# Performance work log

Hardware: AMD Instinct MI355X
Metric: run time of the kernel (lower is better)

The kernel has to match this reference:

```python
import jax, jax.numpy as jnp
import numpy as np

RADIUS = 0.2
MAX_SAMPLES = 32  # max_samples_per_query


def ball_query(coords, queries, radius, k):
    """coords: [B,Np,3], queries: [B,Nq,3] -> idxs: [B,Nq,k] (first-k in index order,
    empty slots filled with the first valid index, or 0 if no neighbor -- matches
    the standard PointNet++ CUDA ball_query semantics)."""
    Np = coords.shape[1]
    # squared distances [B, Nq, Np]
    diff = queries[:, :, None, :] - coords[:, None, :, :]
    d2 = jnp.sum(diff * diff, axis=-1)
    mask = d2 < radius * radius
    # keys: point index if in-ball else sentinel Np; smallest k keys = first k valid indices
    keys = jnp.where(mask, jnp.arange(Np, dtype=jnp.int32), Np)
    neg_top, _ = jax.lax.top_k(-keys, k)           # largest of -keys == smallest keys
    sorted_keys = -neg_top                          # [B, Nq, k], ascending
    valid = sorted_keys < Np
    first = jnp.where(valid[..., 0:1], sorted_keys[..., 0:1], 0)
    return jnp.where(valid, sorted_keys, first)


def setup_inputs() -> dict:
    key = jax.random.key(0)
    k1, k2, k3, k4 = jax.random.split(key, 4)
    B, Np, Nq, C, Ct = 4, 8192, 2048, 64, 64
    return {
        "points_coords": jax.random.uniform(k1, (B, Np, 3), dtype=jnp.float32),
        "points_features": jax.random.normal(k2, (B, C, Np), dtype=jnp.float32),
        "points_t_embed": jax.random.normal(k3, (B, Ct, Np), dtype=jnp.float32),
        "queries": jax.random.uniform(k4, (B, Nq, 3), dtype=jnp.float32),
    }


def reference(points_coords, points_features, points_t_embed, queries):
    B, Np, _ = points_coords.shape
    Nq = queries.shape[1]
    K = MAX_SAMPLES
    idxs = ball_query(points_coords, queries, RADIUS, K)          # [B,Nq,K] int32
    flat = idxs.reshape(B, Nq * K)
    # grouped coords: gather along point dim then center on queries -> [B,Nq,K,3]
    grouped_coords = jnp.take_along_axis(points_coords, flat[:, :, None], axis=1)
    grouped_coords = grouped_coords.reshape(B, Nq, K, 3) - queries[:, :, None, :]
    # grouped features: gather channel-first along point dim -> [B,C,Nq,K]
    C = points_features.shape[1]
    grouped_features = jnp.take_along_axis(points_features, flat[:, None, :], axis=2)
    grouped_features = grouped_features.reshape(B, C, Nq, K)
    # use_coords=True: prepend centered coords as channels
    grouped_features = jnp.concatenate(
        [grouped_coords.transpose(0, 3, 1, 2), grouped_features], axis=1)  # [B,3+C,Nq,K]
    # t_embed gather -> [B,Ct,Nq,K]
    Ct = points_t_embed.shape[1]
    t_embed = jnp.take_along_axis(points_t_embed, flat[:, None, :], axis=2)
    t_embed = t_embed.reshape(B, Ct, Nq, K)
    return grouped_features, t_embed
```

## Files before the change

### kernel.cpp

```cpp
#include <hip/hip_runtime.h>

constexpr int kB  = 4;
constexpr int kNp = 8192;
constexpr int kNq = 2048;
constexpr int kK  = 32;
constexpr float kR2 = (float)(0.2 * 0.2);

typedef float v4f __attribute__((ext_vector_type(4)));
typedef int   v4i __attribute__((ext_vector_type(4)));

__global__ __launch_bounds__(256) void coords_soa_kernel(
    const float* __restrict__ coords, float* __restrict__ cb3)
{
    const int t  = blockIdx.x * 256 + threadIdx.x;
    const int b  = t >> 11;
    const int p4 = t & (kNp / 4 - 1);

    const v4f* c4 = (const v4f*)(coords + (size_t)b * kNp * 3 + (size_t)p4 * 12);
    const v4f d0 = c4[0];
    const v4f d1 = c4[1];
    const v4f d2 = c4[2];

    v4f X = {d0.x, d0.w, d1.z, d2.y};
    v4f Y = {d0.y, d1.x, d1.w, d2.z};
    v4f Z = {d0.z, d1.y, d2.x, d2.w};

    float* o = cb3 + (size_t)b * 3 * kNp;
    ((v4f*)(o + 0 * kNp))[p4] = X;
    ((v4f*)(o + 1 * kNp))[p4] = Y;
    ((v4f*)(o + 2 * kNp))[p4] = Z;
}

__global__ __launch_bounds__(256) void ball_query_kernel(
    const float* __restrict__ cb3,
    const float* __restrict__ queries,
    int* __restrict__ idxs,
    float* __restrict__ out)
{
    const int wave = (int)((blockIdx.x * blockDim.x + threadIdx.x) >> 6);
    const int lane = threadIdx.x & 63;
    const int w    = threadIdx.x >> 6;
    const int b    = wave >> 11;
    const int q    = wave & (kNq - 1);

    const float qx = queries[(b * kNq + q) * 3 + 0];
    const float qy = queries[(b * kNq + q) * 3 + 1];
    const float qz = queries[(b * kNq + q) * 3 + 2];

    const float* __restrict__ cbx = cb3 + (size_t)b * 3 * kNp;
    const float* __restrict__ cby = cbx + kNp;
    const float* __restrict__ cbz = cby + kNp;
    const v4f* __restrict__ cbx4 = (const v4f*)cbx;
    const v4f* __restrict__ cby4 = (const v4f*)cby;
    const v4f* __restrict__ cbz4 = (const v4f*)cbz;

    __shared__ int s_idx[4][kK];

    const unsigned long long lt = (1ull << lane) - 1ull;
    int cnt = 0;

    v4f X = cbx4[lane];
    v4f Y = cby4[lane];
    v4f Z = cbz4[lane];

    for (int base = 0; base < kNp; base += 256) {
        const int nvi = (base + 256 < kNp) ? (((base + 256) >> 2) + lane) : lane;
        const v4f Xn = cbx4[nvi];
        const v4f Yn = cby4[nvi];
        const v4f Zn = cbz4[nvi];

        bool in[4];
        unsigned long long m[4];
#pragma unroll
        for (int j = 0; j < 4; ++j) {
            const float dx = __fsub_rn(qx, X[j]);
            const float dy = __fsub_rn(qy, Y[j]);
            const float dz = __fsub_rn(qz, Z[j]);
            const float d2 = __fadd_rn(
                __fadd_rn(__fmul_rn(dx, dx), __fmul_rn(dy, dy)),
                __fmul_rn(dz, dz));
            in[j] = d2 < kR2;
            m[j] = __ballot(in[j]);
        }

        int pre = cnt + __popcll(m[0] & lt) + __popcll(m[1] & lt)
                      + __popcll(m[2] & lt) + __popcll(m[3] & lt);
        int local = 0;
#pragma unroll
        for (int j = 0; j < 4; ++j) {
            if (in[j]) {
                const int slot = pre + local;
                if (slot < kK) s_idx[w][slot] = base + 4 * lane + j;
                ++local;
            }
        }
        cnt += __popcll(m[0]) + __popcll(m[1])
             + __popcll(m[2]) + __popcll(m[3]);

        X = Xn; Y = Yn; Z = Zn;
        if (cnt >= kK) break;
    }

    if (lane < kK) {
        int v;
        if (cnt == 0)        v = 0;
        else if (lane < cnt) v = s_idx[w][lane];
        else                 v = s_idx[w][0];
        idxs[(size_t)wave * kK + lane] = v;

        const int k = lane;
        float* gf = out + ((size_t)(b * 67) * kNq + q) * kK + k;
        __builtin_nontemporal_store(__fsub_rn(cbx[v], qx), gf + (size_t)0 * kNq * kK);
        __builtin_nontemporal_store(__fsub_rn(cby[v], qy), gf + (size_t)1 * kNq * kK);
        __builtin_nontemporal_store(__fsub_rn(cbz[v], qz), gf + (size_t)2 * kNq * kK);
    }
}

__global__ __launch_bounds__(256) void gather_kernel(
    const float* __restrict__ feat,
    const float* __restrict__ temb,
    const int*   __restrict__ idxs,
    float* __restrict__ out)
{
    const int blk = blockIdx.x;
    const int seg = blk & 1;
    const int bc  = blk >> 1;
    const int b   = bc >> 7;
    const int j   = bc & 127;

    const float* src;
    float* dst;
    if (j < 64) {
        src = feat + ((size_t)b * 64 + j) * kNp;
        dst = out + (size_t)(b * 67 + 3 + j) * (kNq * kK);
    } else {
        src = temb + ((size_t)b * 64 + (j - 64)) * kNp;
        dst = out + (size_t)kB * 67 * kNq * kK
                  + (size_t)(b * 64 + (j - 64)) * (kNq * kK);
    }

    __shared__ float row[kNp];
    {
        const v4f* s4 = (const v4f*)src;
        v4f* r4 = (v4f*)row;
#pragma unroll
        for (int i = 0; i < kNp / 4 / 256; ++i)
            r4[i * 256 + threadIdx.x] = s4[i * 256 + threadIdx.x];
    }
    __syncthreads();

    constexpr int total4 = kNq * kK / 4;
    constexpr int seg4   = total4 / 2;
    const v4i* id4 = (const v4i*)(idxs + (size_t)b * kNq * kK) + seg * seg4;
    v4f* d4 = (v4f*)dst + seg * seg4;
    const int e0 = threadIdx.x;

    v4i id[8];
#pragma unroll
    for (int g = 0; g < 8; ++g)
        id[g] = id4[e0 + g * 256];

#pragma unroll
    for (int pass = 0; pass < 4; ++pass) {
#pragma unroll
        for (int g = 0; g < 8; ++g) {
            const v4i cur = id[g];
            if (pass < 3)
                id[g] = id4[e0 + ((pass + 1) * 8 + g) * 256];
            v4f v;
            v.x = row[cur.x];
            v.y = row[cur.y];
            v.z = row[cur.z];
            v.w = row[cur.w];
            __builtin_nontemporal_store(v, d4 + e0 + (pass * 8 + g) * 256);
        }
    }
}

extern "C" void kernel_launch(void* const* d_in, const int* in_sizes, int n_in,
                              void* d_out, int out_size, void* d_ws, size_t ws_size,
                              hipStream_t stream) {
    const float* coords  = (const float*)d_in[0];
    const float* feats   = (const float*)d_in[1];
    const float* temb    = (const float*)d_in[2];
    const float* queries = (const float*)d_in[3];
    float* out = (float*)d_out;

    int*   idxs = (int*)d_ws;
    float* cb3  = (float*)((char*)d_ws + (size_t)kB * kNq * kK * 4);

    coords_soa_kernel<<<kB * kNp / 4 / 256, 256, 0, stream>>>(coords, cb3);
    ball_query_kernel<<<kB * kNq / 4, 256, 0, stream>>>(cb3, queries, idxs, out);
    gather_kernel<<<kB * 128 * 2, 256, 0, stream>>>(feats, temb, idxs, out);
}
```

Measured before the change: 177.9 us.

## Process two queries per wave and store neighbor indices as 16-bit

Each wavefront now handles two queries, so every loaded batch of point coordinates is tested against both queries, and all 64 lanes write output in the epilogue instead of 32. Neighbor indices shrink from int32 to uint16, since Np=8192 fits in 16 bits. This halves index traffic between the ball-query and gather kernels, and the gather unpacks two indices per 32-bit word. The costs are half as many ball-query waves and a loop that runs until the slower of the two queries fills its 32 neighbors.

```diff
diff --git a/kernel.cpp b/kernel.cpp
--- a/kernel.cpp
+++ b/kernel.cpp
@@ -6,8 +6,9 @@
 constexpr int kK  = 32;
 constexpr float kR2 = (float)(0.2 * 0.2);
 
-typedef float v4f __attribute__((ext_vector_type(4)));
-typedef int   v4i __attribute__((ext_vector_type(4)));
+typedef float        v4f __attribute__((ext_vector_type(4)));
+typedef int          v4i __attribute__((ext_vector_type(4)));
+typedef unsigned int v2u __attribute__((ext_vector_type(2)));
 
 __global__ __launch_bounds__(256) void coords_soa_kernel(
     const float* __restrict__ coords, float* __restrict__ cb3)
@@ -34,18 +35,18 @@
 __global__ __launch_bounds__(256) void ball_query_kernel(
     const float* __restrict__ cb3,
     const float* __restrict__ queries,
-    int* __restrict__ idxs,
+    unsigned short* __restrict__ idxs,
     float* __restrict__ out)
 {
-    const int wave = (int)((blockIdx.x * blockDim.x + threadIdx.x) >> 6);
+    const int wq   = (int)((blockIdx.x * blockDim.x + threadIdx.x) >> 6);
     const int lane = threadIdx.x & 63;
     const int w    = threadIdx.x >> 6;
-    const int b    = wave >> 11;
-    const int q    = wave & (kNq - 1);
-
-    const float qx = queries[(b * kNq + q) * 3 + 0];
-    const float qy = queries[(b * kNq + q) * 3 + 1];
-    const float qz = queries[(b * kNq + q) * 3 + 2];
+    const int b    = wq >> 10;
+    const int qa   = (wq & (kNq / 2 - 1)) * 2;
+
+    const float* qp = queries + ((size_t)b * kNq + qa) * 3;
+    const float qx0 = qp[0], qy0 = qp[1], qz0 = qp[2];
+    const float qx1 = qp[3], qy1 = qp[4], qz1 = qp[5];
 
     const float* __restrict__ cbx = cb3 + (size_t)b * 3 * kNp;
     const float* __restrict__ cby = cbx + kNp;
@@ -54,10 +55,10 @@
     const v4f* __restrict__ cby4 = (const v4f*)cby;
     const v4f* __restrict__ cbz4 = (const v4f*)cbz;
 
-    __shared__ int s_idx[4][kK];
+    __shared__ int s_idx[4][2][kK];
 
     const unsigned long long lt = (1ull << lane) - 1ull;
-    int cnt = 0;
+    int cnt0 = 0, cnt1 = 0;
 
     v4f X = cbx4[lane];
     v4f Y = cby4[lane];
@@ -69,57 +70,91 @@
         const v4f Yn = cby4[nvi];
         const v4f Zn = cbz4[nvi];
 
-        bool in[4];
-        unsigned long long m[4];
-#pragma unroll
-        for (int j = 0; j < 4; ++j) {
-            const float dx = __fsub_rn(qx, X[j]);
-            const float dy = __fsub_rn(qy, Y[j]);
-            const float dz = __fsub_rn(qz, Z[j]);
-            const float d2 = __fadd_rn(
-                __fadd_rn(__fmul_rn(dx, dx), __fmul_rn(dy, dy)),
-                __fmul_rn(dz, dz));
-            in[j] = d2 < kR2;
-            m[j] = __ballot(in[j]);
+        if (cnt0 < kK) {
+            bool in[4];
+            unsigned long long m[4];
+#pragma unroll
+            for (int j = 0; j < 4; ++j) {
+                const float dx = __fsub_rn(qx0, X[j]);
+                const float dy = __fsub_rn(qy0, Y[j]);
+                const float dz = __fsub_rn(qz0, Z[j]);
+                const float d2 = __fadd_rn(
+                    __fadd_rn(__fmul_rn(dx, dx), __fmul_rn(dy, dy)),
+                    __fmul_rn(dz, dz));
+                in[j] = d2 < kR2;
+                m[j] = __ballot(in[j]);
+            }
+            int pre = cnt0 + __popcll(m[0] & lt) + __popcll(m[1] & lt)
+                           + __popcll(m[2] & lt) + __popcll(m[3] & lt);
+            int local = 0;
+#pragma unroll
+            for (int j = 0; j < 4; ++j) {
+                if (in[j]) {
+                    const int slot = pre + local;
+                    if (slot < kK) s_idx[w][0][slot] = base + 4 * lane + j;
+                    ++local;
+                }
+            }
+            cnt0 += __popcll(m[0]) + __popcll(m[1])
+                  + __popcll(m[2]) + __popcll(m[3]);
         }
 
-        int pre = cnt + __popcll(m[0] & lt) + __popcll(m[1] & lt)
-                      + __popcll(m[2] & lt) + __popcll(m[3] & lt);
-        int local = 0;
-#pragma unroll
-        for (int j = 0; j < 4; ++j) {
-            if (in[j]) {
-                const int slot = pre + local;
-                if (slot < kK) s_idx[w][slot] = base + 4 * lane + j;
-                ++local;
-            }
+        if (cnt1 < kK) {
+            bool in[4];
+            unsigned long long m[4];
+#pragma unroll
+            for (int j = 0; j < 4; ++j) {
+                const float dx = __fsub_rn(qx1, X[j]);
+                const float dy = __fsub_rn(qy1, Y[j]);
+                const float dz = __fsub_rn(qz1, Z[j]);
+                const float d2 = __fadd_rn(
+                    __fadd_rn(__fmul_rn(dx, dx), __fmul_rn(dy, dy)),
+                    __fmul_rn(dz, dz));
+                in[j] = d2 < kR2;
+                m[j] = __ballot(in[j]);
+            }
+            int pre = cnt1 + __popcll(m[0] & lt) + __popcll(m[1] & lt)
+                           + __popcll(m[2] & lt) + __popcll(m[3] & lt);
+            int local = 0;
+#pragma unroll
+            for (int j = 0; j < 4; ++j) {
+                if (in[j]) {
+                    const int slot = pre + local;
+                    if (slot < kK) s_idx[w][1][slot] = base + 4 * lane + j;
+                    ++local;
+                }
+            }
+            cnt1 += __popcll(m[0]) + __popcll(m[1])
+                  + __popcll(m[2]) + __popcll(m[3]);
         }
-        cnt += __popcll(m[0]) + __popcll(m[1])
-             + __popcll(m[2]) + __popcll(m[3]);
 
         X = Xn; Y = Yn; Z = Zn;
-        if (cnt >= kK) break;
-    }
-
-    if (lane < kK) {
-        int v;
-        if (cnt == 0)        v = 0;
-        else if (lane < cnt) v = s_idx[w][lane];
-        else                 v = s_idx[w][0];
-        idxs[(size_t)wave * kK + lane] = v;
-
-        const int k = lane;
-        float* gf = out + ((size_t)(b * 67) * kNq + q) * kK + k;
-        __builtin_nontemporal_store(__fsub_rn(cbx[v], qx), gf + (size_t)0 * kNq * kK);
-        __builtin_nontemporal_store(__fsub_rn(cby[v], qy), gf + (size_t)1 * kNq * kK);
-        __builtin_nontemporal_store(__fsub_rn(cbz[v], qz), gf + (size_t)2 * kNq * kK);
-    }
+        if (cnt0 >= kK && cnt1 >= kK) break;
+    }
+
+    const int half = lane >> 5;
+    const int k    = lane & (kK - 1);
+    const int cnt  = half ? cnt1 : cnt0;
+    int v;
+    if (cnt == 0)     v = 0;
+    else if (k < cnt) v = s_idx[w][half][k];
+    else              v = s_idx[w][half][0];
+
+    idxs[((size_t)(b * kNq + qa)) * kK + lane] = (unsigned short)v;
+
+    const float qxh = half ? qx1 : qx0;
+    const float qyh = half ? qy1 : qy0;
+    const float qzh = half ? qz1 : qz0;
+    float* gf = out + ((size_t)(b * 67) * kNq + qa) * kK + lane;
+    __builtin_nontemporal_store(__fsub_rn(cbx[v], qxh), gf + (size_t)0 * kNq * kK);
+    __builtin_nontemporal_store(__fsub_rn(cby[v], qyh), gf + (size_t)1 * kNq * kK);
+    __builtin_nontemporal_store(__fsub_rn(cbz[v], qzh), gf + (size_t)2 * kNq * kK);
 }
 
 __global__ __launch_bounds__(256) void gather_kernel(
     const float* __restrict__ feat,
     const float* __restrict__ temb,
-    const int*   __restrict__ idxs,
+    const unsigned short* __restrict__ idxs,
     float* __restrict__ out)
 {
     const int blk = blockIdx.x;
@@ -151,27 +186,27 @@
 
     constexpr int total4 = kNq * kK / 4;
     constexpr int seg4   = total4 / 2;
-    const v4i* id4 = (const v4i*)(idxs + (size_t)b * kNq * kK) + seg * seg4;
+    const v2u* id2 = (const v2u*)(idxs + (size_t)b * kNq * kK) + seg * seg4;
     v4f* d4 = (v4f*)dst + seg * seg4;
     const int e0 = threadIdx.x;
 
-    v4i id[8];
+    v2u id[8];
 #pragma unroll
     for (int g = 0; g < 8; ++g)
-        id[g] = id4[e0 + g * 256];
+        id[g] = id2[e0 + g * 256];
 
 #pragma unroll
     for (int pass = 0; pass < 4; ++pass) {
 #pragma unroll
         for (int g = 0; g < 8; ++g) {
-            const v4i cur = id[g];
+            const v2u cur = id[g];
             if (pass < 3)
-                id[g] = id4[e0 + ((pass + 1) * 8 + g) * 256];
+                id[g] = id2[e0 + ((pass + 1) * 8 + g) * 256];
             v4f v;
-            v.x = row[cur.x];
-            v.y = row[cur.y];
-            v.z = row[cur.z];
-            v.w = row[cur.w];
+            v.x = row[cur.x & 0xffffu];
+            v.y = row[cur.x >> 16];
+            v.z = row[cur.y & 0xffffu];
+            v.w = row[cur.y >> 16];
             __builtin_nontemporal_store(v, d4 + e0 + (pass * 8 + g) * 256);
         }
     }
@@ -186,10 +221,10 @@
     const float* queries = (const float*)d_in[3];
     float* out = (float*)d_out;
 
-    int*   idxs = (int*)d_ws;
-    float* cb3  = (float*)((char*)d_ws + (size_t)kB * kNq * kK * 4);
+    unsigned short* idxs = (unsigned short*)d_ws;
+    float* cb3 = (float*)((char*)d_ws + (size_t)kB * kNq * kK * 2);
 
     coords_soa_kernel<<<kB * kNp / 4 / 256, 256, 0, stream>>>(coords, cb3);
-    ball_query_kernel<<<kB * kNq / 4, 256, 0, stream>>>(cb3, queries, idxs, out);
+    ball_query_kernel<<<kB * kNq / 8, 256, 0, stream>>>(cb3, queries, idxs, out);
     gather_kernel<<<kB * 128 * 2, 256, 0, stream>>>(feats, temb, idxs, out);
 }
```

Result: no change. 177.3 us (-0.3%).
